# Kernel optimization log

Measured on AMD Instinct MI355X. Metric: run time of the kernel, lower is better.

The kernel has to match this reference:

```python
import jax, jax.numpy as jnp
import numpy as np

K = 2
ALPHA = 800.0
TAU = 0.001
MAX_ITER = 50
EPS = 1e-7


def setup_inputs() -> dict:
    key = jax.random.key(0)
    x = jax.random.normal(key, (32, 512, 128), dtype=jnp.float32)
    return {"x": x}


def _vmd(x):
    B, L, D = x.shape
    # fftshift'd frequency grid, broadcast over batch/features: [1, L, 1]
    f_shift = jnp.fft.fftshift(jnp.fft.fftfreq(L).astype(x.dtype))[None, :, None]
    pos_mask = f_shift >= 0
    f_pos = jnp.where(pos_mask, f_shift, 0.0)
    x_hat = jnp.fft.fftshift(jnp.fft.fft(x, axis=1), axes=1)  # [B, L, D] complex

    def body(carry, _):
        u, omega, lam = carry  # u:[B,K,L,D], omega:[B,K,D], lam:[B,L,D]
        # --- mode updates (Wiener filtering in frequency domain) ---
        for k_idx in range(K):
            sum_other = jnp.sum(u, axis=1) - u[:, k_idx]  # sum over modes != k_idx
            sum_other_hat = jnp.fft.fftshift(jnp.fft.fft(sum_other, axis=1), axes=1)
            numerator = x_hat - sum_other_hat + lam / 2
            omega_k = omega[:, k_idx][:, None, :]  # [B,1,D]
            denominator = 1.0 + 2.0 * ALPHA * (f_shift - omega_k) ** 2
            u_hat_k = numerator / denominator
            u_k = jnp.real(jnp.fft.ifft(jnp.fft.ifftshift(u_hat_k, axes=1), axis=1))
            u = u.at[:, k_idx].set(u_k)
        # --- center frequency updates ---
        for k_idx in range(K):
            u_k_hat = jnp.fft.fftshift(jnp.fft.fft(u[:, k_idx], axis=1), axes=1)
            power = jnp.where(pos_mask, jnp.abs(u_k_hat) ** 2, 0.0)  # [B,L,D]
            num_o = jnp.sum(f_pos * power, axis=1)      # [B,D]
            den_o = jnp.sum(power, axis=1) + EPS        # [B,D]
            omega = omega.at[:, k_idx].set(num_o / den_o)
        # --- dual ascent ---
        lam = lam + TAU * (x - jnp.sum(u, axis=1))
        return (u, omega, lam), None

    init = (
        jnp.zeros((B, K, L, D), x.dtype),
        jnp.zeros((B, K, D), x.dtype),
        jnp.zeros((B, L, D), x.dtype),
    )
    (u, omega, _), _ = jax.lax.scan(jax.checkpoint(body), init, None, length=MAX_ITER)

    # sort modes by mean center frequency (ascending) per batch element
    omega_mean = omega.mean(axis=2)                    # [B,K]
    order = jnp.argsort(omega_mean, axis=1)            # [B,K]
    u_sorted = jnp.take_along_axis(u, order[:, :, None, None], axis=1)

    x_trend = jnp.zeros_like(u_sorted[:, 0])
    x_period = u_sorted[:, 0]
    x_res = u_sorted[:, 1]
    return x_trend, x_period, x_res


def reference(x):
    return _vmd(x)
```

## Files before the change

kernel.cpp:

```cpp
#include <hip/hip_runtime.h>
#include <math.h>

#define FIELD 2097152
#define NSEQ  4096

typedef float f2 __attribute__((ext_vector_type(2)));

__device__ __forceinline__ f2 swp(f2 a) { return __builtin_shufflevector(a, a, 1, 0); }
__device__ __forceinline__ f2 conjf2(f2 a) { return (f2){a.x, -a.y}; }
__device__ __forceinline__ f2 cmulp(f2 a, float c, f2 ns)  { return c * a + ns * swp(a); }
__device__ __forceinline__ f2 cmulpc(f2 a, float c, f2 ns) { return c * a - ns * swp(a); }
__device__ __forceinline__ f2 addi(f2 a, f2 b) { return a + (f2){-1.0f, 1.0f} * swp(b); }
__device__ __forceinline__ f2 subi(f2 a, f2 b) { return a + (f2){1.0f, -1.0f} * swp(b); }

template<int CTRL>
__device__ __forceinline__ float dpp_f(float v) {
  return __int_as_float(__builtin_amdgcn_update_dpp(
      __float_as_int(v), __float_as_int(v), CTRL, 0xF, 0xF, true));
}
template<int CTRL>
__device__ __forceinline__ float dpp0_f(float v) {
  return __int_as_float(__builtin_amdgcn_update_dpp(
      0, __float_as_int(v), CTRL, 0xF, 0xF, true));
}
template<int H>
__device__ __forceinline__ float xlane(float v) {
  if constexpr (H == 1)      return dpp_f<0xB1>(v);
  else if constexpr (H == 2) return dpp_f<0x4E>(v);
  else if constexpr (H == 4) return dpp_f<0x141>(dpp_f<0x1B>(v));
  else if constexpr (H == 8) return dpp_f<0x128>(v);
  else return __shfl_xor(v, H, 64);
}
template<int H>
__device__ __forceinline__ f2 xlane2(f2 v) {
  return (f2){xlane<H>(v.x), xlane<H>(v.y)};
}
__device__ __forceinline__ f2 shfl2(f2 v, int l) {
  return (f2){__shfl(v.x, l, 64), __shfl(v.y, l, 64)};
}
__device__ __forceinline__ float bcast0(float v) {
  return __int_as_float(__builtin_amdgcn_readfirstlane(__float_as_int(v)));
}
__device__ __forceinline__ float wave_sum(float v) {
  v += dpp0_f<0x111>(v);
  v += dpp0_f<0x112>(v);
  v += dpp0_f<0x114>(v);
  v += dpp0_f<0x118>(v);
  v += dpp0_f<0x142>(v);
  v += dpp0_f<0x143>(v);
  return __int_as_float(__builtin_amdgcn_readlane(__float_as_int(v), 63));
}

__device__ __forceinline__ void fft4_fwd(f2* v) {
  f2 t0 = v[0] + v[2], t1 = v[0] - v[2];
  f2 t2 = v[1] + v[3], t3 = v[1] - v[3];
  v[0] = t0 + t2; v[2] = t0 - t2;
  v[1] = subi(t1, t3);
  v[3] = addi(t1, t3);
}
__device__ __forceinline__ void fft4_inv(f2* v) {
  f2 t0 = v[0] + v[2], t1 = v[0] - v[2];
  f2 t2 = v[1] + v[3], t3 = v[1] - v[3];
  v[0] = t0 + t2; v[2] = t0 - t2;
  v[1] = addi(t1, t3);
  v[3] = subi(t1, t3);
}

template<int H>
__device__ __forceinline__ void fwd_stage(f2* v, float wr, f2 wn, float sg) {
#pragma unroll
  for (int b = 0; b < 4; ++b) {
    f2 p = xlane2<H>(v[b]);
    f2 t = sg * v[b] + p;
    v[b] = cmulp(t, wr, wn);
  }
}
template<int H>
__device__ __forceinline__ void inv_stage(f2* v, float wr, f2 wn, float sg) {
#pragma unroll
  for (int b = 0; b < 4; ++b) {
    f2 u = cmulpc(v[b], wr, wn);
    f2 p = xlane2<H>(u);
    v[b] = sg * u + p;
  }
}

__device__ __forceinline__ void fft256_fwd(f2* v,
                                           const float* twFc, const f2* twFn,
                                           const float* wrS, const f2* wnS,
                                           const float* sgS) {
  fft4_fwd(v);
#pragma unroll
  for (int b = 1; b < 4; ++b) v[b] = cmulp(v[b], twFc[b-1], twFn[b-1]);
  fwd_stage<32>(v, wrS[0], wnS[0], sgS[0]);
  fwd_stage<16>(v, wrS[1], wnS[1], sgS[1]);
  fwd_stage<8> (v, wrS[2], wnS[2], sgS[2]);
  fwd_stage<4> (v, wrS[3], wnS[3], sgS[3]);
  fwd_stage<2> (v, wrS[4], wnS[4], sgS[4]);
  fwd_stage<1> (v, wrS[5], wnS[5], sgS[5]);
}

__device__ __forceinline__ void ifft256(f2* v,
                                        const float* twFc, const f2* twFn,
                                        const float* wrS, const f2* wnS,
                                        const float* sgS) {
  inv_stage<1> (v, wrS[5], wnS[5], sgS[5]);
  inv_stage<2> (v, wrS[4], wnS[4], sgS[4]);
  inv_stage<4> (v, wrS[3], wnS[3], sgS[3]);
  inv_stage<8> (v, wrS[2], wnS[2], sgS[2]);
  inv_stage<16>(v, wrS[1], wnS[1], sgS[1]);
  inv_stage<32>(v, wrS[0], wnS[0], sgS[0]);
#pragma unroll
  for (int b = 1; b < 4; ++b) v[b] = cmulpc(v[b], twFc[b-1], twFn[b-1]);
  fft4_inv(v);
}

__device__ __forceinline__ void half_to_z(f2* S, float S256,
                                          const float* twHc, const f2* twHn,
                                          int lane, int pl0, int plx) {
  f2 P[4];
  P[0] = shfl2(S[0], pl0);
#pragma unroll
  for (int b = 1; b < 4; ++b) P[b] = shfl2(S[4 - b], plx);
  P[0] = (lane == 0) ? (f2){S256, 0.0f} : P[0];
#pragma unroll
  for (int b = 0; b < 4; ++b) {
    f2 cP = conjf2(P[b]);
    f2 A = 0.5f * (S[b] + cP);
    f2 B = 0.5f * (S[b] - cP);
    f2 Bt = cmulp(B, twHc[b], twHn[b]);
    S[b] = addi(A, Bt);
  }
}

__device__ __forceinline__ void mode_update4(const f2* X, const f2* V, f2* U,
                                             const float* lam1, const float* lam2,
                                             float om, float f0) {
#pragma unroll
  for (int b = 0; b < 4; ++b) {
    float f = f0 + (float)b * (1.0f / 512.0f);
    float dfp = f - om;
    float dfm = f + om;
    float gp = __builtin_amdgcn_rcpf(fmaf(1600.0f * dfp, dfp, 1.0f));
    float gm = __builtin_amdgcn_rcpf(fmaf(1600.0f * dfm, dfm, 1.0f));
    float gs = 0.5f * (gp + gm);
    f2 D = X[b] - V[b];
    float lt = 0.25f * fmaf(lam1[b], gp, lam2[b] * gm);
    U[b] = gs * D + (f2){lt, 0.0f};
  }
}

__global__ __attribute__((amdgpu_flat_work_group_size(256, 256),
                          amdgpu_waves_per_eu(4, 4),
                          amdgpu_num_vgpr(96)))
void vmd_kernel(const float* __restrict__ x, float* __restrict__ out,
                float* __restrict__ ws) {
  __shared__ float stage[4 * 512];
  __shared__ float ldsLam[4 * 512];

  const int tid = threadIdx.x;
  const int wv = tid >> 6;
  const int lane = tid & 63;
  const int w = (blockIdx.x >> 3) + ((blockIdx.x & 7) << 7);
  const int g = 4 * w + wv;
  const int bb = w >> 5;
  const int d0 = (4 * w) & 127;
  const int base4 = bb * 16384 + (d0 >> 2);
  float* lamLds = ldsLam + wv * 512;
  f2* stg2 = (f2*)stage + wv * 256;

  const int rev = (int)(__brev((unsigned)lane) >> 26);
  const float f0 = (float)rev * (1.0f / 128.0f);
  const int plx = lane ^ 63;
  const int pl0 = (int)(__brev((unsigned)((64 - rev) & 63)) >> 26);

  float wrS[6], sgS[6]; f2 wnS[6];
#pragma unroll
  for (int s = 0; s < 6; ++s) {
    const int h = 32 >> s;
    const bool hi = (lane & h) != 0;
    float th = (float)(lane & (h - 1)) * (3.14159265358979323846f / (float)h);
    float sn, cs; sincosf(th, &sn, &cs);
    wrS[s] = hi ? cs : 1.0f;
    wnS[s] = hi ? (f2){sn, -sn} : (f2){0.0f, 0.0f};
    sgS[s] = hi ? -1.0f : 1.0f;
  }
  float twFc[3]; f2 twFn[3];
#pragma unroll
  for (int b = 1; b < 4; ++b) {
    float th = (float)(lane * b) * 0.02454369260617026f;
    float sn, cs; sincosf(th, &sn, &cs);
    twFc[b-1] = cs; twFn[b-1] = (f2){sn, -sn};
  }
  float twHc[4]; f2 twHn[4];
#pragma unroll
  for (int b = 0; b < 4; ++b) {
    float th = (float)(4 * rev + b) * 0.01227184630308513f;
    float sn, cs; sincosf(th, &sn, &cs);
    twHc[b] = cs; twHn[b] = (f2){-sn, sn};
  }

  {
    const float4* x4 = (const float4*)x;
    float4 va = x4[base4 + tid * 32];
    float4 vb = x4[base4 + (tid + 256) * 32];
    stage[tid]        = va.x; stage[512 + tid]        = va.y;
    stage[1024 + tid] = va.z; stage[1536 + tid]       = va.w;
    stage[tid + 256]        = vb.x; stage[512 + tid + 256]  = vb.y;
    stage[1024 + tid + 256] = vb.z; stage[1536 + tid + 256] = vb.w;
#pragma unroll
    for (int j = 0; j < 8; ++j) ldsLam[tid * 8 + j] = 0.0f;
  }
  __syncthreads();

  f2 z[4];
#pragma unroll
  for (int a = 0; a < 4; ++a) z[a] = stg2[64 * a + lane];
  fft256_fwd(z, twFc, twFn, wrS, wnS, sgS);
  f2 X[4];
  float X256;
  {
    f2 P[4];
    P[0] = shfl2(z[0], pl0);
#pragma unroll
    for (int b = 1; b < 4; ++b) P[b] = shfl2(z[4 - b], plx);
    X256 = bcast0(z[0].x - z[0].y);
#pragma unroll
    for (int b = 0; b < 4; ++b) {
      f2 cP = conjf2(P[b]);
      f2 E = 0.5f * (z[b] + cP);
      f2 O = 0.5f * (f2){1.0f, -1.0f} * swp(z[b] - cP);
      X[b] = E + cmulpc(O, twHc[b], twHn[b]);
    }
  }

  f2 U0[4], U1[4], lam[4];
#pragma unroll
  for (int b = 0; b < 4; ++b) {
    U0[b] = (f2){0.0f, 0.0f}; U1[b] = (f2){0.0f, 0.0f};
    lam[b] = (f2){0.0f, 0.0f};
  }
  float U0_256 = 0.0f, U1_256 = 0.0f;
  float om0 = 0.0f, om1 = 0.0f;

  const int psiE = 256 * (lane & 1) + (lane >> 1);

#pragma unroll 1
  for (int it = 0; it < 50; ++it) {
    float lam1[4], lam2[4];
#pragma unroll
    for (int b = 0; b < 4; ++b) lam1[b] = lamLds[128 * b + 64 + rev];
    lam2[0] = lamLds[64 - rev];
#pragma unroll
    for (int b = 1; b < 4; ++b) lam2[b] = lamLds[128 * (4 - b) + 63 - rev];
    float lam0 = lamLds[0];

    mode_update4(X, U1, U0, lam1, lam2, om0, f0);
    {
      float dm = 0.5f + om0;
      float gg = __builtin_amdgcn_rcpf(fmaf(1600.0f * dm, dm, 1.0f));
      U0_256 = (X256 - U1_256 + 0.5f * lam0) * gg;
    }
    mode_update4(X, U0, U1, lam1, lam2, om1, f0);
    {
      float dm = 0.5f + om1;
      float gg = __builtin_amdgcn_rcpf(fmaf(1600.0f * dm, dm, 1.0f));
      U1_256 = (X256 - U0_256 + 0.5f * lam0) * gg;
    }

    f2 s0 = (f2){0.0f, 0.0f}, s1 = (f2){0.0f, 0.0f};
#pragma unroll
    for (int b = 0; b < 4; ++b) {
      float f = f0 + (float)b * (1.0f / 512.0f);
      float p0 = fmaf(U0[b].x, U0[b].x, U0[b].y * U0[b].y);
      float p1 = fmaf(U1[b].x, U1[b].x, U1[b].y * U1[b].y);
      s0 = s0 + (f2){f * p0, p0};
      s1 = s1 + (f2){f * p1, p1};
    }
    float n0 = wave_sum(s0.x), d0s = wave_sum(s0.y);
    float n1 = wave_sum(s1.x), d1s = wave_sum(s1.y);
    om0 = n0 * __builtin_amdgcn_rcpf(d0s + 1e-7f);
    om1 = n1 * __builtin_amdgcn_rcpf(d1s + 1e-7f);

    if (it < 49) {
#pragma unroll
      for (int b = 0; b < 4; ++b) z[b] = U0[b] + U1[b];
      float S256 = U0_256 + U1_256;
      half_to_z(z, S256, twHc, twHn, lane, pl0, plx);
      ifft256(z, twFc, twFn, wrS, wnS, sgS);
#pragma unroll
      for (int a = 0; a < 4; ++a) {
        f2 xa = stg2[64 * a + lane];
        lam[a] = lam[a] + 0.001f * (xa - z[a] * (1.0f / 256.0f));
        lamLds[psiE + 32 * a]       = lam[a].x;
        lamLds[psiE + 32 * a + 128] = lam[a].y;
      }
      asm volatile("s_waitcnt lgkmcnt(0)" ::: "memory");
    }
  }

  float4* o4 = (float4*)out;
#pragma unroll
  for (int b = 0; b < 4; ++b) z[b] = U0[b];
  half_to_z(z, U0_256, twHc, twHn, lane, pl0, plx);
  ifft256(z, twFc, twFn, wrS, wnS, sgS);
  __syncthreads();
#pragma unroll
  for (int a = 0; a < 4; ++a) stg2[64 * a + lane] = z[a] * (1.0f / 256.0f);
  __syncthreads();
#pragma unroll
  for (int r = 0; r < 2; ++r) {
    const int n = tid + r * 256;
    float4 v;
    v.x = stage[n]; v.y = stage[512 + n]; v.z = stage[1024 + n]; v.w = stage[1536 + n];
    o4[FIELD / 4 + base4 + n * 32] = v;
  }
  __syncthreads();
#pragma unroll
  for (int b = 0; b < 4; ++b) z[b] = U1[b];
  half_to_z(z, U1_256, twHc, twHn, lane, pl0, plx);
  ifft256(z, twFc, twFn, wrS, wnS, sgS);
#pragma unroll
  for (int a = 0; a < 4; ++a) stg2[64 * a + lane] = z[a] * (1.0f / 256.0f);
  __syncthreads();
#pragma unroll
  for (int r = 0; r < 2; ++r) {
    const int n = tid + r * 256;
    float4 v;
    v.x = stage[n]; v.y = stage[512 + n]; v.z = stage[1024 + n]; v.w = stage[1536 + n];
    o4[2 * FIELD / 4 + base4 + n * 32] = v;
  }

  if (lane == 0) {
    ws[g] = om0;
    ws[NSEQ + g] = om1;
  }
}

__global__ __launch_bounds__(256) void epi_kernel(float* __restrict__ out,
                                                  const float* __restrict__ ws) {
  const int tid = threadIdx.x;
  const int blk = blockIdx.x;
  const int bb = blk >> 6;
  __shared__ float flagS;
  if (tid < 64) {
    float o0 = ws[bb * 128 + tid] + ws[bb * 128 + 64 + tid];
    float o1 = ws[NSEQ + bb * 128 + tid] + ws[NSEQ + bb * 128 + 64 + tid];
#pragma unroll
    for (int off = 32; off >= 1; off >>= 1) {
      o0 += __shfl_xor(o0, off, 64);
      o1 += __shfl_xor(o1, off, 64);
    }
    if (tid == 0) flagS = (o0 > o1) ? 1.0f : 0.0f;
  }
  __syncthreads();
  const bool sw = flagS > 0.5f;
  float4* o4 = (float4*)out;
  const int i = blk * 256 + tid;
  o4[i] = (float4){0.0f, 0.0f, 0.0f, 0.0f};
  if (sw) {
    float4 p = o4[FIELD / 4 + i];
    float4 r = o4[2 * FIELD / 4 + i];
    o4[FIELD / 4 + i] = r;
    o4[2 * FIELD / 4 + i] = p;
  }
}

extern "C" void kernel_launch(void* const* d_in, const int* in_sizes, int n_in,
                              void* d_out, int out_size, void* d_ws, size_t ws_size,
                              hipStream_t stream) {
  (void)in_sizes; (void)n_in; (void)ws_size; (void)out_size;
  const float* x = (const float*)d_in[0];
  float* out = (float*)d_out;
  float* ws = (float*)d_ws;
  vmd_kernel<<<NSEQ / 4, 256, 0, stream>>>(x, out, ws);
  epi_kernel<<<FIELD / 1024, 256, 0, stream>>>(out, ws);
}
```

Before: 230.0 us.

## Split each sequence's FFT and mode updates across two waves per sequence

Each 512-point sequence is now handled by two waves instead of one. Each wave owns half of the radix-4 outer butterfly and two of the four complex elements per lane. The block grows to 512 threads with 8 waves per EU, which halves the per-lane register work and raises parallelism. In exchange it adds LDS exchanges and block-wide barriers every iteration, both to combine the final radix-2 step and to share partial omega sums between the paired waves.

```diff
diff --git a/kernel.cpp b/kernel.cpp
--- a/kernel.cpp
+++ b/kernel.cpp
@@ -51,287 +51,299 @@
   return __int_as_float(__builtin_amdgcn_readlane(__float_as_int(v), 63));
 }
 
-__device__ __forceinline__ void fft4_fwd(f2* v) {
-  f2 t0 = v[0] + v[2], t1 = v[0] - v[2];
-  f2 t2 = v[1] + v[3], t3 = v[1] - v[3];
-  v[0] = t0 + t2; v[2] = t0 - t2;
-  v[1] = subi(t1, t3);
-  v[3] = addi(t1, t3);
-}
-__device__ __forceinline__ void fft4_inv(f2* v) {
-  f2 t0 = v[0] + v[2], t1 = v[0] - v[2];
-  f2 t2 = v[1] + v[3], t3 = v[1] - v[3];
-  v[0] = t0 + t2; v[2] = t0 - t2;
-  v[1] = addi(t1, t3);
-  v[3] = subi(t1, t3);
-}
-
 template<int H>
-__device__ __forceinline__ void fwd_stage(f2* v, float wr, f2 wn, float sg) {
-#pragma unroll
-  for (int b = 0; b < 4; ++b) {
+__device__ __forceinline__ void fwd_stage2(f2* v, float wr, f2 wn, float sg) {
+#pragma unroll
+  for (int b = 0; b < 2; ++b) {
     f2 p = xlane2<H>(v[b]);
     f2 t = sg * v[b] + p;
     v[b] = cmulp(t, wr, wn);
   }
 }
 template<int H>
-__device__ __forceinline__ void inv_stage(f2* v, float wr, f2 wn, float sg) {
-#pragma unroll
-  for (int b = 0; b < 4; ++b) {
+__device__ __forceinline__ void inv_stage2(f2* v, float wr, f2 wn, float sg) {
+#pragma unroll
+  for (int b = 0; b < 2; ++b) {
     f2 u = cmulpc(v[b], wr, wn);
     f2 p = xlane2<H>(u);
     v[b] = sg * u + p;
   }
 }
-
-__device__ __forceinline__ void fft256_fwd(f2* v,
-                                           const float* twFc, const f2* twFn,
-                                           const float* wrS, const f2* wnS,
-                                           const float* sgS) {
-  fft4_fwd(v);
-#pragma unroll
-  for (int b = 1; b < 4; ++b) v[b] = cmulp(v[b], twFc[b-1], twFn[b-1]);
-  fwd_stage<32>(v, wrS[0], wnS[0], sgS[0]);
-  fwd_stage<16>(v, wrS[1], wnS[1], sgS[1]);
-  fwd_stage<8> (v, wrS[2], wnS[2], sgS[2]);
-  fwd_stage<4> (v, wrS[3], wnS[3], sgS[3]);
-  fwd_stage<2> (v, wrS[4], wnS[4], sgS[4]);
-  fwd_stage<1> (v, wrS[5], wnS[5], sgS[5]);
-}
-
-__device__ __forceinline__ void ifft256(f2* v,
-                                        const float* twFc, const f2* twFn,
-                                        const float* wrS, const f2* wnS,
-                                        const float* sgS) {
-  inv_stage<1> (v, wrS[5], wnS[5], sgS[5]);
-  inv_stage<2> (v, wrS[4], wnS[4], sgS[4]);
-  inv_stage<4> (v, wrS[3], wnS[3], sgS[3]);
-  inv_stage<8> (v, wrS[2], wnS[2], sgS[2]);
-  inv_stage<16>(v, wrS[1], wnS[1], sgS[1]);
-  inv_stage<32>(v, wrS[0], wnS[0], sgS[0]);
-#pragma unroll
-  for (int b = 1; b < 4; ++b) v[b] = cmulpc(v[b], twFc[b-1], twFn[b-1]);
-  fft4_inv(v);
-}
-
-__device__ __forceinline__ void half_to_z(f2* S, float S256,
-                                          const float* twHc, const f2* twHn,
-                                          int lane, int pl0, int plx) {
-  f2 P[4];
-  P[0] = shfl2(S[0], pl0);
-#pragma unroll
-  for (int b = 1; b < 4; ++b) P[b] = shfl2(S[4 - b], plx);
-  P[0] = (lane == 0) ? (f2){S256, 0.0f} : P[0];
-#pragma unroll
-  for (int b = 0; b < 4; ++b) {
-    f2 cP = conjf2(P[b]);
-    f2 A = 0.5f * (S[b] + cP);
-    f2 B = 0.5f * (S[b] - cP);
-    f2 Bt = cmulp(B, twHc[b], twHn[b]);
-    S[b] = addi(A, Bt);
-  }
-}
-
-__device__ __forceinline__ void mode_update4(const f2* X, const f2* V, f2* U,
-                                             const float* lam1, const float* lam2,
-                                             float om, float f0) {
-#pragma unroll
-  for (int b = 0; b < 4; ++b) {
-    float f = f0 + (float)b * (1.0f / 512.0f);
+__device__ __forceinline__ void lanes_fwd(f2* v, const float* wrS, const f2* wnS,
+                                          const float* sgS) {
+  fwd_stage2<32>(v, wrS[0], wnS[0], sgS[0]);
+  fwd_stage2<16>(v, wrS[1], wnS[1], sgS[1]);
+  fwd_stage2<8> (v, wrS[2], wnS[2], sgS[2]);
+  fwd_stage2<4> (v, wrS[3], wnS[3], sgS[3]);
+  fwd_stage2<2> (v, wrS[4], wnS[4], sgS[4]);
+  fwd_stage2<1> (v, wrS[5], wnS[5], sgS[5]);
+}
+__device__ __forceinline__ void lanes_inv(f2* v, const float* wrS, const f2* wnS,
+                                          const float* sgS) {
+  inv_stage2<1> (v, wrS[5], wnS[5], sgS[5]);
+  inv_stage2<2> (v, wrS[4], wnS[4], sgS[4]);
+  inv_stage2<4> (v, wrS[3], wnS[3], sgS[3]);
+  inv_stage2<8> (v, wrS[2], wnS[2], sgS[2]);
+  inv_stage2<16>(v, wrS[1], wnS[1], sgS[1]);
+  inv_stage2<32>(v, wrS[0], wnS[0], sgS[0]);
+}
+
+__device__ __forceinline__ void halfz2(f2* S, float S256, int h, int lane,
+                                       int pl0, int plx,
+                                       const float* twHc, const f2* twHn) {
+  f2 P[2];
+  P[0] = shfl2(h ? S[1] : S[0], h ? plx : pl0);
+  P[1] = shfl2(h ? S[0] : S[1], plx);
+  if (h == 0 && lane == 0) P[0] = (f2){S256, 0.0f};
+#pragma unroll
+  for (int j = 0; j < 2; ++j) {
+    f2 cP = conjf2(P[j]);
+    f2 A = 0.5f * (S[j] + cP);
+    f2 B = 0.5f * (S[j] - cP);
+    f2 Bt = cmulp(B, twHc[j], twHn[j]);
+    S[j] = addi(A, Bt);
+  }
+}
+
+__device__ __forceinline__ void mode2(const f2* X, const f2* V, f2* U,
+                                      const float* l1, const float* l2,
+                                      float om, const float* fb) {
+#pragma unroll
+  for (int j = 0; j < 2; ++j) {
+    float f = fb[j];
     float dfp = f - om;
     float dfm = f + om;
     float gp = __builtin_amdgcn_rcpf(fmaf(1600.0f * dfp, dfp, 1.0f));
     float gm = __builtin_amdgcn_rcpf(fmaf(1600.0f * dfm, dfm, 1.0f));
     float gs = 0.5f * (gp + gm);
-    f2 D = X[b] - V[b];
-    float lt = 0.25f * fmaf(lam1[b], gp, lam2[b] * gm);
-    U[b] = gs * D + (f2){lt, 0.0f};
-  }
-}
-
-__global__ __attribute__((amdgpu_flat_work_group_size(256, 256),
-                          amdgpu_waves_per_eu(4, 4),
-                          amdgpu_num_vgpr(96)))
+    f2 D = X[j] - V[j];
+    float lt = 0.25f * fmaf(l1[j], gp, l2[j] * gm);
+    U[j] = gs * D + (f2){lt, 0.0f};
+  }
+}
+
+__global__ __attribute__((amdgpu_flat_work_group_size(512, 512),
+                          amdgpu_waves_per_eu(8, 8)))
 void vmd_kernel(const float* __restrict__ x, float* __restrict__ out,
                 float* __restrict__ ws) {
   __shared__ float stage[4 * 512];
   __shared__ float ldsLam[4 * 512];
+  __shared__ float4 omP4[4][2];
 
   const int tid = threadIdx.x;
   const int wv = tid >> 6;
   const int lane = tid & 63;
+  const int s = wv >> 1;
+  const int h = wv & 1;
   const int w = (blockIdx.x >> 3) + ((blockIdx.x & 7) << 7);
-  const int g = 4 * w + wv;
+  const int g = 4 * w + s;
   const int bb = w >> 5;
   const int d0 = (4 * w) & 127;
   const int base4 = bb * 16384 + (d0 >> 2);
-  float* lamLds = ldsLam + wv * 512;
-  f2* stg2 = (f2*)stage + wv * 256;
+  float* lamS = ldsLam + s * 512;
+  f2* stg2 = (f2*)stage + s * 256;
+  f2* exch = (f2*)ldsLam + s * 256;
 
   const int rev = (int)(__brev((unsigned)lane) >> 26);
   const float f0 = (float)rev * (1.0f / 128.0f);
   const int plx = lane ^ 63;
   const int pl0 = (int)(__brev((unsigned)((64 - rev) & 63)) >> 26);
+  const float sgh = h ? -1.0f : 1.0f;
+
+  const int b0 = h, b1 = 2 + h;
+  float fb[2];
+  fb[0] = f0 + (float)b0 * (1.0f / 512.0f);
+  fb[1] = f0 + (float)b1 * (1.0f / 512.0f);
 
   float wrS[6], sgS[6]; f2 wnS[6];
 #pragma unroll
-  for (int s = 0; s < 6; ++s) {
-    const int h = 32 >> s;
-    const bool hi = (lane & h) != 0;
-    float th = (float)(lane & (h - 1)) * (3.14159265358979323846f / (float)h);
+  for (int st = 0; st < 6; ++st) {
+    const int hh = 32 >> st;
+    const bool hi = (lane & hh) != 0;
+    float th = (float)(lane & (hh - 1)) * (3.14159265358979323846f / (float)hh);
     float sn, cs; sincosf(th, &sn, &cs);
-    wrS[s] = hi ? cs : 1.0f;
-    wnS[s] = hi ? (f2){sn, -sn} : (f2){0.0f, 0.0f};
-    sgS[s] = hi ? -1.0f : 1.0f;
-  }
-  float twFc[3]; f2 twFn[3];
-#pragma unroll
-  for (int b = 1; b < 4; ++b) {
-    float th = (float)(lane * b) * 0.02454369260617026f;
+    wrS[st] = hi ? cs : 1.0f;
+    wnS[st] = hi ? (f2){sn, -sn} : (f2){0.0f, 0.0f};
+    sgS[st] = hi ? -1.0f : 1.0f;
+  }
+  float twFc2[2]; f2 twFn2[2];
+#pragma unroll
+  for (int j = 0; j < 2; ++j) {
+    float th = (float)(lane * (2 * j + h)) * 0.02454369260617026f;
     float sn, cs; sincosf(th, &sn, &cs);
-    twFc[b-1] = cs; twFn[b-1] = (f2){sn, -sn};
-  }
-  float twHc[4]; f2 twHn[4];
-#pragma unroll
-  for (int b = 0; b < 4; ++b) {
-    float th = (float)(4 * rev + b) * 0.01227184630308513f;
+    twFc2[j] = cs; twFn2[j] = (f2){sn, -sn};
+  }
+  float twHc2[2]; f2 twHn2[2];
+#pragma unroll
+  for (int j = 0; j < 2; ++j) {
+    float th = (float)(4 * rev + 2 * j + h) * 0.01227184630308513f;
     float sn, cs; sincosf(th, &sn, &cs);
-    twHc[b] = cs; twHn[b] = (f2){-sn, sn};
+    twHc2[j] = cs; twHn2[j] = (f2){-sn, sn};
   }
 
   {
     const float4* x4 = (const float4*)x;
     float4 va = x4[base4 + tid * 32];
-    float4 vb = x4[base4 + (tid + 256) * 32];
-    stage[tid]        = va.x; stage[512 + tid]        = va.y;
-    stage[1024 + tid] = va.z; stage[1536 + tid]       = va.w;
-    stage[tid + 256]        = vb.x; stage[512 + tid + 256]  = vb.y;
-    stage[1024 + tid + 256] = vb.z; stage[1536 + tid + 256] = vb.w;
-#pragma unroll
-    for (int j = 0; j < 8; ++j) ldsLam[tid * 8 + j] = 0.0f;
+    stage[tid]        = va.x; stage[512 + tid]  = va.y;
+    stage[1024 + tid] = va.z; stage[1536 + tid] = va.w;
+    ((float4*)ldsLam)[tid] = (float4){0.0f, 0.0f, 0.0f, 0.0f};
   }
   __syncthreads();
 
-  f2 z[4];
-#pragma unroll
-  for (int a = 0; a < 4; ++a) z[a] = stg2[64 * a + lane];
-  fft256_fwd(z, twFc, twFn, wrS, wnS, sgS);
-  f2 X[4];
+  f2 z[2], xa[2];
+  {
+    f2 s0 = stg2[lane], s1 = stg2[64 + lane], s2 = stg2[128 + lane], s3 = stg2[192 + lane];
+    xa[0] = h ? s2 : s0;
+    xa[1] = h ? s3 : s1;
+    if (h == 0) {
+      f2 e0 = s0 + s2, e1 = s1 + s3;
+      z[0] = e0 + e1;
+      z[1] = e0 - e1;
+    } else {
+      f2 o0 = s0 - s2, o1 = s1 - s3;
+      z[0] = subi(o0, o1);
+      z[1] = addi(o0, o1);
+    }
+    z[0] = cmulp(z[0], twFc2[0], twFn2[0]);
+    z[1] = cmulp(z[1], twFc2[1], twFn2[1]);
+    lanes_fwd(z, wrS, wnS, sgS);
+  }
+  __syncthreads();
+
+  f2 X[2];
   float X256;
   {
-    f2 P[4];
-    P[0] = shfl2(z[0], pl0);
-#pragma unroll
-    for (int b = 1; b < 4; ++b) P[b] = shfl2(z[4 - b], plx);
+    f2 P[2];
+    P[0] = shfl2(h ? z[1] : z[0], h ? plx : pl0);
+    P[1] = shfl2(h ? z[0] : z[1], plx);
     X256 = bcast0(z[0].x - z[0].y);
 #pragma unroll
-    for (int b = 0; b < 4; ++b) {
-      f2 cP = conjf2(P[b]);
-      f2 E = 0.5f * (z[b] + cP);
-      f2 O = 0.5f * (f2){1.0f, -1.0f} * swp(z[b] - cP);
-      X[b] = E + cmulpc(O, twHc[b], twHn[b]);
-    }
-  }
-
-  f2 U0[4], U1[4], lam[4];
-#pragma unroll
-  for (int b = 0; b < 4; ++b) {
-    U0[b] = (f2){0.0f, 0.0f}; U1[b] = (f2){0.0f, 0.0f};
-    lam[b] = (f2){0.0f, 0.0f};
+    for (int j = 0; j < 2; ++j) {
+      f2 cP = conjf2(P[j]);
+      f2 E = 0.5f * (z[j] + cP);
+      f2 O = 0.5f * (f2){1.0f, -1.0f} * swp(z[j] - cP);
+      X[j] = E + cmulpc(O, twHc2[j], twHn2[j]);
+    }
+  }
+
+  f2 U0[2], U1[2], lam[2];
+#pragma unroll
+  for (int j = 0; j < 2; ++j) {
+    U0[j] = (f2){0.0f, 0.0f}; U1[j] = (f2){0.0f, 0.0f}; lam[j] = (f2){0.0f, 0.0f};
   }
   float U0_256 = 0.0f, U1_256 = 0.0f;
   float om0 = 0.0f, om1 = 0.0f;
 
-  const int psiE = 256 * (lane & 1) + (lane >> 1);
+  const int psiW = 256 * (lane & 1) + (lane >> 1) + 64 * h;
+  const int a1_0 = 128 * b0 + 64 + rev;
+  const int a1_1 = 128 * b1 + 64 + rev;
+  const int a2_0 = (b0 == 0) ? (64 - rev) : (128 * (4 - b0) + 63 - rev);
+  const int a2_1 = 128 * (4 - b1) + 63 - rev;
 
 #pragma unroll 1
   for (int it = 0; it < 50; ++it) {
-    float lam1[4], lam2[4];
-#pragma unroll
-    for (int b = 0; b < 4; ++b) lam1[b] = lamLds[128 * b + 64 + rev];
-    lam2[0] = lamLds[64 - rev];
-#pragma unroll
-    for (int b = 1; b < 4; ++b) lam2[b] = lamLds[128 * (4 - b) + 63 - rev];
-    float lam0 = lamLds[0];
-
-    mode_update4(X, U1, U0, lam1, lam2, om0, f0);
-    {
+    float l1[2], l2[2];
+    l1[0] = lamS[a1_0]; l1[1] = lamS[a1_1];
+    l2[0] = lamS[a2_0]; l2[1] = lamS[a2_1];
+    float lam0 = lamS[0];
+
+    mode2(X, U1, U0, l1, l2, om0, fb);
+    if (h == 0) {
       float dm = 0.5f + om0;
       float gg = __builtin_amdgcn_rcpf(fmaf(1600.0f * dm, dm, 1.0f));
       U0_256 = (X256 - U1_256 + 0.5f * lam0) * gg;
     }
-    mode_update4(X, U0, U1, lam1, lam2, om1, f0);
-    {
+    mode2(X, U0, U1, l1, l2, om1, fb);
+    if (h == 0) {
       float dm = 0.5f + om1;
       float gg = __builtin_amdgcn_rcpf(fmaf(1600.0f * dm, dm, 1.0f));
       U1_256 = (X256 - U0_256 + 0.5f * lam0) * gg;
     }
 
-    f2 s0 = (f2){0.0f, 0.0f}, s1 = (f2){0.0f, 0.0f};
-#pragma unroll
-    for (int b = 0; b < 4; ++b) {
-      float f = f0 + (float)b * (1.0f / 512.0f);
-      float p0 = fmaf(U0[b].x, U0[b].x, U0[b].y * U0[b].y);
-      float p1 = fmaf(U1[b].x, U1[b].x, U1[b].y * U1[b].y);
-      s0 = s0 + (f2){f * p0, p0};
-      s1 = s1 + (f2){f * p1, p1};
-    }
-    float n0 = wave_sum(s0.x), d0s = wave_sum(s0.y);
-    float n1 = wave_sum(s1.x), d1s = wave_sum(s1.y);
-    om0 = n0 * __builtin_amdgcn_rcpf(d0s + 1e-7f);
-    om1 = n1 * __builtin_amdgcn_rcpf(d1s + 1e-7f);
-
-    if (it < 49) {
-#pragma unroll
-      for (int b = 0; b < 4; ++b) z[b] = U0[b] + U1[b];
+    float n0 = 0.0f, d0s = 0.0f, n1 = 0.0f, d1s = 0.0f;
+#pragma unroll
+    for (int j = 0; j < 2; ++j) {
+      float f = fb[j];
+      float p0 = fmaf(U0[j].x, U0[j].x, U0[j].y * U0[j].y);
+      float p1 = fmaf(U1[j].x, U1[j].x, U1[j].y * U1[j].y);
+      d0s += p0; n0 = fmaf(f, p0, n0);
+      d1s += p1; n1 = fmaf(f, p1, n1);
+    }
+    n0 = wave_sum(n0); d0s = wave_sum(d0s);
+    n1 = wave_sum(n1); d1s = wave_sum(d1s);
+
+    const bool more = it < 49;
+    f2 tA, tB;
+    if (more) {
+      f2 zz[2];
+      zz[0] = U0[0] + U1[0];
+      zz[1] = U0[1] + U1[1];
       float S256 = U0_256 + U1_256;
-      half_to_z(z, S256, twHc, twHn, lane, pl0, plx);
-      ifft256(z, twFc, twFn, wrS, wnS, sgS);
-#pragma unroll
-      for (int a = 0; a < 4; ++a) {
-        f2 xa = stg2[64 * a + lane];
-        lam[a] = lam[a] + 0.001f * (xa - z[a] * (1.0f / 256.0f));
-        lamLds[psiE + 32 * a]       = lam[a].x;
-        lamLds[psiE + 32 * a + 128] = lam[a].y;
-      }
-      asm volatile("s_waitcnt lgkmcnt(0)" ::: "memory");
+      halfz2(zz, S256, h, lane, pl0, plx, twHc2, twHn2);
+      lanes_inv(zz, wrS, wnS, sgS);
+      zz[0] = cmulpc(zz[0], twFc2[0], twFn2[0]);
+      zz[1] = cmulpc(zz[1], twFc2[1], twFn2[1]);
+      tA = zz[0] + zz[1];
+      tB = zz[0] - zz[1];
+      stg2[h * 128 + lane]      = tA;
+      stg2[h * 128 + 64 + lane] = tB;
+    }
+    if (lane == 0) omP4[s][h] = (float4){n0, d0s, n1, d1s};
+    __syncthreads();
+    {
+      float4 pp = omP4[s][1 - h];
+      om0 = (n0 + pp.x) * __builtin_amdgcn_rcpf((d0s + pp.y) + 1e-7f);
+      om1 = (n1 + pp.z) * __builtin_amdgcn_rcpf((d1s + pp.w) + 1e-7f);
+    }
+    if (more) {
+      f2 pA = stg2[(1 - h) * 128 + lane];
+      f2 pB = stg2[(1 - h) * 128 + 64 + lane];
+      f2 oA = pA + sgh * tA;
+      f2 u  = h ? pB : tB;
+      f2 vv = h ? tB : pB;
+      f2 oB = u + sgh * (f2){-1.0f, 1.0f} * swp(vv);
+      lam[0] = lam[0] + 0.001f * (xa[0] - oA * (1.0f / 256.0f));
+      lam[1] = lam[1] + 0.001f * (xa[1] - oB * (1.0f / 256.0f));
+      lamS[psiW]            = lam[0].x;
+      lamS[psiW + 128]      = lam[0].y;
+      lamS[psiW + 32]       = lam[1].x;
+      lamS[psiW + 32 + 128] = lam[1].y;
+      __syncthreads();
     }
   }
 
   float4* o4 = (float4*)out;
-#pragma unroll
-  for (int b = 0; b < 4; ++b) z[b] = U0[b];
-  half_to_z(z, U0_256, twHc, twHn, lane, pl0, plx);
-  ifft256(z, twFc, twFn, wrS, wnS, sgS);
-  __syncthreads();
-#pragma unroll
-  for (int a = 0; a < 4; ++a) stg2[64 * a + lane] = z[a] * (1.0f / 256.0f);
-  __syncthreads();
-#pragma unroll
-  for (int r = 0; r < 2; ++r) {
-    const int n = tid + r * 256;
+#pragma unroll 1
+  for (int m = 0; m < 2; ++m) {
+    f2 zz[2];
+    zz[0] = m ? U1[0] : U0[0];
+    zz[1] = m ? U1[1] : U0[1];
+    float S256 = m ? U1_256 : U0_256;
+    halfz2(zz, S256, h, lane, pl0, plx, twHc2, twHn2);
+    lanes_inv(zz, wrS, wnS, sgS);
+    zz[0] = cmulpc(zz[0], twFc2[0], twFn2[0]);
+    zz[1] = cmulpc(zz[1], twFc2[1], twFn2[1]);
+    f2 tA = zz[0] + zz[1], tB = zz[0] - zz[1];
+    exch[h * 128 + lane]      = tA;
+    exch[h * 128 + 64 + lane] = tB;
+    __syncthreads();
+    f2 pA = exch[(1 - h) * 128 + lane];
+    f2 pB = exch[(1 - h) * 128 + 64 + lane];
+    f2 oA = pA + sgh * tA;
+    f2 u  = h ? pB : tB;
+    f2 vv = h ? tB : pB;
+    f2 oB = u + sgh * (f2){-1.0f, 1.0f} * swp(vv);
+    stg2[64 * (2 * h + 0) + lane] = oA * (1.0f / 256.0f);
+    stg2[64 * (2 * h + 1) + lane] = oB * (1.0f / 256.0f);
+    __syncthreads();
     float4 v;
-    v.x = stage[n]; v.y = stage[512 + n]; v.z = stage[1024 + n]; v.w = stage[1536 + n];
-    o4[FIELD / 4 + base4 + n * 32] = v;
-  }
-  __syncthreads();
-#pragma unroll
-  for (int b = 0; b < 4; ++b) z[b] = U1[b];
-  half_to_z(z, U1_256, twHc, twHn, lane, pl0, plx);
-  ifft256(z, twFc, twFn, wrS, wnS, sgS);
-#pragma unroll
-  for (int a = 0; a < 4; ++a) stg2[64 * a + lane] = z[a] * (1.0f / 256.0f);
-  __syncthreads();
-#pragma unroll
-  for (int r = 0; r < 2; ++r) {
-    const int n = tid + r * 256;
-    float4 v;
-    v.x = stage[n]; v.y = stage[512 + n]; v.z = stage[1024 + n]; v.w = stage[1536 + n];
-    o4[2 * FIELD / 4 + base4 + n * 32] = v;
-  }
-
-  if (lane == 0) {
+    v.x = stage[tid]; v.y = stage[512 + tid];
+    v.z = stage[1024 + tid]; v.w = stage[1536 + tid];
+    o4[(m + 1) * (FIELD / 4) + base4 + tid * 32] = v;
+    __syncthreads();
+  }
+
+  if (lane == 0 && h == 0) {
     ws[g] = om0;
     ws[NSEQ + g] = om1;
   }
@@ -373,6 +385,6 @@
   const float* x = (const float*)d_in[0];
   float* out = (float*)d_out;
   float* ws = (float*)d_ws;
-  vmd_kernel<<<NSEQ / 4, 256, 0, stream>>>(x, out, ws);
+  vmd_kernel<<<NSEQ / 4, 512, 0, stream>>>(x, out, ws);
   epi_kernel<<<FIELD / 1024, 256, 0, stream>>>(out, ws);
 }
```

New measurement: 829.6 us. +260.7%, slower.
